# Performance work log

Hardware: AMD Instinct MI355X
Metric: run time of the kernel (lower is better)

Reference implementation:

```python
import jax, jax.numpy as jnp
import numpy as np

EDGE_TYPES = 7
TIME_STEP = 5
STATE_DIM = 1024


def setup_inputs() -> dict:
    key = jax.random.key(0)
    ks = jax.random.split(key, 8)
    B, T, N, DF = 4, 15, 15, 25600
    S, E = STATE_DIM, EDGE_TYPES
    # weights ~ N(0, 0.01), biases zero, matching _initialization()
    return {
        "pose_features": jax.random.normal(ks[0], (B, T, N, DF), jnp.float32),
        "W_compress": jax.random.normal(ks[1], (DF, S), jnp.float32) * 0.01,
        "b_compress": jnp.zeros((S,), jnp.float32),
        "W_edge": jax.random.normal(ks[2], (E, S, S), jnp.float32) * 0.01,
        "b_edge": jnp.zeros((E, S), jnp.float32),
        "W_att": jax.random.normal(ks[3], (E, 2 * S), jnp.float32) * 0.01,
        "b_att": jnp.zeros((E,), jnp.float32),
        "W_r": jax.random.normal(ks[4], (2 * S, S), jnp.float32) * 0.01,
        "b_r": jnp.zeros((S,), jnp.float32),
        "W_z": jax.random.normal(ks[5], (2 * S, S), jnp.float32) * 0.01,
        "b_z": jnp.zeros((S,), jnp.float32),
        "W_h": jax.random.normal(ks[6], (2 * S, S), jnp.float32) * 0.01,
        "b_h": jnp.zeros((S,), jnp.float32),
    }


def reference(pose_features, W_compress, b_compress, W_edge, b_edge,
              W_att, b_att, W_r, b_r, W_z, b_z, W_h, b_h):
    B, T, N, DF = pose_features.shape
    S = W_compress.shape[1]
    E = W_edge.shape[0]
    x = pose_features.reshape(B * T, N, DF)
    prop = x @ W_compress + b_compress                      # [M, N, S]
    # attention Linear over concat(row, col) == row-part + col-part (rank-1 broadcast,
    # avoids materializing the [M, N, N, 2S] repeat/cat tensor; identical math)
    Wa_row, Wa_col = W_att[:, :S], W_att[:, S:]
    scores = None
    for _ in range(1 + TIME_STEP):
        msg = jnp.einsum('bnd,edh->benh', prop, W_edge) + b_edge[None, :, None, :]  # [M,E,N,S]
        row = jnp.einsum('bend,ed->ben', msg, Wa_row)       # [M, E, N]
        col = jnp.einsum('bend,ed->ben', msg, Wa_col)
        scores = jax.nn.sigmoid(row[..., :, None] + col[..., None, :]
                                + b_att[None, :, None, None])   # [M, E, N, N]
        merged = jnp.einsum('beij,bejd->bid', scores, msg)  # [M, N, S]
        a = jnp.concatenate([merged, prop], axis=-1)        # [M, N, 2S]
        r = jax.nn.sigmoid(a @ W_r + b_r)
        z = jax.nn.sigmoid(a @ W_z + b_z)
        h_hat = jnp.tanh(jnp.concatenate([merged, r * prop], axis=-1) @ W_h + b_h)
        prop = (1 - z) * prop + z * h_hat
    box_states = scores.transpose(0, 2, 3, 1)               # [M, N, N, E]
    action_score = ((1 - box_states[..., 0:1]) * box_states).sum(axis=2)
    action_score = action_score.reshape(B, T, N, E)
    actor_score = (1 - box_states[..., 0]).reshape(B, T, N, N)
    acty_score = jax.nn.softmax(
        (action_score * actor_score.sum(axis=-1)[..., None]).sum(axis=2)[:, :, 1:],
        axis=-1)
    return action_score, acty_score, actor_score
```

## Files before the change

kernel.cpp:

```cpp
#include <hip/hip_runtime.h>
#include <hip/hip_bf16.h>

typedef unsigned short bf16_t;
typedef __bf16 bf16x8 __attribute__((ext_vector_type(8)));
typedef float f32x4 __attribute__((ext_vector_type(4)));

__device__ __forceinline__ unsigned short f2bf(float x){
  union { __hip_bfloat16 h; unsigned short u; } c;
  c.h = __float2bfloat16(x);
  return c.u;
}
__device__ __forceinline__ float bf2f(bf16_t u){
  union { unsigned short u; __hip_bfloat16 h; } c;
  c.u = u;
  return __bfloat162float(c.h);
}

#define GL2L(g, l) __builtin_amdgcn_global_load_lds( \
    (const __attribute__((address_space(1))) unsigned int*)(g), \
    (__attribute__((address_space(3))) unsigned int*)(l), 16, 0, 0)

template<int ACT, int MAP>
__global__ __launch_bounds__(256)
void gemm_bf16(const bf16_t* __restrict__ A, int lda,
               const bf16_t* __restrict__ Bt, int ldb,
               float* __restrict__ C, int ldc, size_t csplit,
               const float* __restrict__ bias,
               int M, int N, int K, int Kchunk)
{
  __shared__ __align__(16) bf16_t As[3][128*32];
  __shared__ __align__(16) bf16_t Bs[3][128*32];
  const int tid = threadIdx.x;
  const int w = tid >> 6, lane = tid & 63;
  const int wm = w >> 1, wn = w & 1;
  const int lr = lane & 15, kq = lane >> 4;
  int bcol, brow, bks;
  if (MAP == 0) { bcol = blockIdx.x; brow = blockIdx.y; bks = blockIdx.z; }
  else          { bks = blockIdx.x;  bcol = blockIdx.y; brow = blockIdx.z; }
  const int gm0 = brow * 128, gn0 = bcol * 128;
  const int k0 = bks * Kchunk;
  const int nt = (min(k0 + Kchunk, K) - k0) >> 5;

  const int srow = lane >> 2;
  const int scol = ((lane & 3) ^ ((srow >> 1) & 3)) << 3;
  const int am0 = min(gm0 + w*32 + srow,      M-1);
  const int am1 = min(gm0 + w*32 + 16 + srow, M-1);
  const int bn0 = min(gn0 + w*32 + srow,      N-1);
  const int bn1 = min(gn0 + w*32 + 16 + srow, N-1);
  const bf16_t* Ag0 = A  + (size_t)am0*lda + scol;
  const bf16_t* Ag1 = A  + (size_t)am1*lda + scol;
  const bf16_t* Bg0 = Bt + (size_t)bn0*ldb + scol;
  const bf16_t* Bg1 = Bt + (size_t)bn1*ldb + scol;

  auto STAGEF = [&](int t, int slot) {
    const int kk = k0 + (t << 5);
    char* al = (char*)(&As[slot][0]) + w*2048;
    char* bl = (char*)(&Bs[slot][0]) + w*2048;
    GL2L(Ag0 + kk, al);
    GL2L(Ag1 + kk, al + 1024);
    GL2L(Bg0 + kk, bl);
    GL2L(Bg1 + kk, bl + 1024);
  };

  STAGEF(0, 0);
  if (nt > 1) STAGEF(1, 1);

  const int kqs = kq ^ ((lr >> 1) & 3);
  f32x4 acc[4][4] = {};

  int cs = 0;
  for (int t = 0; t < nt; ++t) {
    if (nt - t >= 2) { asm volatile("s_waitcnt vmcnt(4)" ::: "memory"); }
    else             { asm volatile("s_waitcnt vmcnt(0)" ::: "memory"); }
    __builtin_amdgcn_s_barrier();
    __builtin_amdgcn_sched_barrier(0);
    if (t + 2 < nt) {
      const int s2 = (cs >= 1) ? cs - 1 : cs + 2;
      STAGEF(t + 2, s2);
    }
    const char* Ab = (const char*)(&As[cs][0]);
    const char* Bb = (const char*)(&Bs[cs][0]);
    bf16x8 af[4], bfr[4];
#pragma unroll
    for (int mi = 0; mi < 4; mi++)
      af[mi] = *(const bf16x8*)(Ab + ((wm*64 + mi*16 + lr) << 6) + (kqs << 4));
#pragma unroll
    for (int ni = 0; ni < 4; ni++)
      bfr[ni] = *(const bf16x8*)(Bb + ((wn*64 + ni*16 + lr) << 6) + (kqs << 4));
    __builtin_amdgcn_s_setprio(1);
#pragma unroll
    for (int mi = 0; mi < 4; mi++)
#pragma unroll
      for (int ni = 0; ni < 4; ni++)
        acc[mi][ni] = __builtin_amdgcn_mfma_f32_16x16x32_bf16(af[mi], bfr[ni], acc[mi][ni], 0, 0, 0);
    __builtin_amdgcn_s_setprio(0);
    __builtin_amdgcn_sched_barrier(0);
    cs = (cs == 2) ? 0 : cs + 1;
  }

#pragma unroll
  for (int mi = 0; mi < 4; mi++) {
#pragma unroll
    for (int ni = 0; ni < 4; ni++) {
      const int col = gn0 + wn*64 + ni*16 + lr;
      const float bv = (ACT == 4) ? bias[col] : 0.f;
#pragma unroll
      for (int i = 0; i < 4; i++) {
        const int row = gm0 + wm*64 + mi*16 + kq*4 + i;
        if (row < M) {
          const float v = acc[mi][ni][i] + bv;
          if (ACT == 4) ((bf16_t*)C)[(size_t)row*ldc + col] = f2bf(v);
          else C[(size_t)bks*csplit + (size_t)row*ldc + col] = v;
        }
      }
    }
  }
}

__global__ void reduce_compress(const float* __restrict__ part, const float* __restrict__ bias,
                                float* __restrict__ prop, bf16_t* __restrict__ xr)
{
  const int idx = blockIdx.x*256 + threadIdx.x;
  const int m = idx >> 10, d = idx & 1023;
  float v = bias[d];
#pragma unroll
  for (int z = 0; z < 8; z++) v += part[(size_t)z*921600 + idx];
  prop[idx] = v;
  xr[(size_t)m*2048 + 1024 + d] = f2bf(v);
}

__global__ void reduce_rz(const float* __restrict__ part, const float* __restrict__ bias,
                          const float* __restrict__ prop, float* __restrict__ Zbuf,
                          bf16_t* __restrict__ Xh)
{
  const int idx = blockIdx.x*256 + threadIdx.x;
  const int m = idx >> 11, c = idx & 2047;
  float v = part[idx] + part[1843200 + idx] + bias[c];
  v = 1.f / (1.f + __expf(-v));
  if (c < 1024) Xh[(size_t)m*2048 + 1024 + c] = f2bf(v * prop[(size_t)m*1024 + c]);
  else          Zbuf[(size_t)m*1024 + (c - 1024)] = v;
}

__global__ void reduce_h(const float* __restrict__ part, const float* __restrict__ bias,
                         const float* __restrict__ Zbuf, float* __restrict__ prop,
                         bf16_t* __restrict__ X)
{
  const int idx = blockIdx.x*256 + threadIdx.x;
  const int m = idx >> 10, d = idx & 1023;
  float v = bias[d];
#pragma unroll
  for (int z = 0; z < 4; z++) v += part[(size_t)z*921600 + idx];
  v = tanhf(v);
  const float zz = Zbuf[idx];
  const float pn = (1.f - zz)*prop[idx] + zz*v;
  prop[idx] = pn;
  X[(size_t)m*2048 + 1024 + d] = f2bf(pn);
}

__global__ void compute_u(const float* __restrict__ We, const float* __restrict__ Wa,
                          float* __restrict__ u_row, float* __restrict__ u_col)
{
  const int w = threadIdx.x >> 6, lane = threadIdx.x & 63;
  const int idx = blockIdx.x*4 + w;
  const int e = idx >> 10, h = idx & 1023;
  const float* wep = We + ((size_t)e*1024 + h)*1024;
  const float* wr  = Wa + (size_t)e*2048;
  const float* wc  = wr + 1024;
  float ar = 0.f, ac = 0.f;
#pragma unroll
  for (int t = 0; t < 16; t++) {
    const float v = wep[lane + 64*t];
    ar += v*wr[lane + 64*t];
    ac += v*wc[lane + 64*t];
  }
  for (int off = 32; off; off >>= 1) { ar += __shfl_down(ar, off); ac += __shfl_down(ac, off); }
  if (lane == 0) { u_row[idx] = ar; u_col[idx] = ac; }
}

__global__ void crc_kernel(const float* __restrict__ be, const float* __restrict__ Wa,
                           float* __restrict__ crc)
{
  const int w = threadIdx.x >> 6, lane = threadIdx.x & 63;
  for (int idx = w; idx < 14; idx += 4) {
    const int e = idx >> 1, which = idx & 1;
    const float* bp = be + e*1024;
    const float* wp = Wa + (size_t)e*2048 + which*1024;
    float a = 0.f;
#pragma unroll
    for (int t = 0; t < 16; t++) a += bp[lane + 64*t]*wp[lane + 64*t];
    for (int off = 32; off; off >>= 1) a += __shfl_down(a, off);
    if (lane == 0) crc[which*7 + e] = a;
  }
}

__global__ void attn_kernel(const float* __restrict__ prop, const float* __restrict__ u_row,
                            const float* __restrict__ u_col, const float* __restrict__ crc,
                            const float* __restrict__ b_att, float* __restrict__ scores)
{
  const int b = blockIdx.x, e = blockIdx.y;
  __shared__ float rowv[15], colv[15];
  const int w = threadIdx.x >> 6, lane = threadIdx.x & 63;
  const float* ur = u_row + (size_t)e*1024;
  const float* uc = u_col + (size_t)e*1024;
  for (int n = w; n < 15; n += 4) {
    const float* pr = prop + (size_t)(b*15 + n)*1024;
    float ar = 0.f, ac = 0.f;
#pragma unroll
    for (int t = 0; t < 16; t++) {
      const float pv = pr[lane + 64*t];
      ar += pv*ur[lane + 64*t];
      ac += pv*uc[lane + 64*t];
    }
    for (int off = 32; off; off >>= 1) { ar += __shfl_down(ar, off); ac += __shfl_down(ac, off); }
    if (lane == 0) { rowv[n] = ar; colv[n] = ac; }
  }
  __syncthreads();
  const float base = b_att[e] + crc[e] + crc[7 + e];
  for (int idx = threadIdx.x; idx < 225; idx += 256) {
    const int i = idx/15, j = idx - i*15;
    const float s = 1.f / (1.f + __expf(-(rowv[i] + colv[j] + base)));
    scores[((size_t)(b*7 + e)*15 + i)*15 + j] = s;
  }
}

__global__ void merged_kernel(const bf16_t* __restrict__ msg, const float* __restrict__ scores,
                              bf16_t* __restrict__ X, bf16_t* __restrict__ Xh)
{
  const int b = blockIdx.x, c = blockIdx.y;
  __shared__ float ms[15*7*128];
  __shared__ float sc[1575];
  for (int q = threadIdx.x; q < 3360; q += 256) {
    const int idx = q*4;
    const int j = idx / 896;
    const int rem = idx - j*896;
    const int e = rem >> 7, dl = rem & 127;
    const ushort4 v = *(const ushort4*)(msg + (size_t)(b*15 + j)*7168 + e*1024 + c*128 + dl);
    ms[idx]   = bf2f(v.x);
    ms[idx+1] = bf2f(v.y);
    ms[idx+2] = bf2f(v.z);
    ms[idx+3] = bf2f(v.w);
  }
  for (int idx = threadIdx.x; idx < 1575; idx += 256)
    sc[idx] = scores[(size_t)b*1575 + idx];
  __syncthreads();
  for (int oi = threadIdx.x; oi < 1920; oi += 256) {
    const int i = oi >> 7, dl = oi & 127;
    float acc = 0.f;
#pragma unroll
    for (int e = 0; e < 7; e++)
#pragma unroll
      for (int j = 0; j < 15; j++)
        acc += sc[(e*15 + i)*15 + j] * ms[j*896 + e*128 + dl];
    const bf16_t o = f2bf(acc);
    X [(size_t)(b*15 + i)*2048 + c*128 + dl] = o;
    Xh[(size_t)(b*15 + i)*2048 + c*128 + dl] = o;
  }
}

__global__ void transpose_k(const float* __restrict__ in, bf16_t* __restrict__ out,
                            int R, int C, int out_ld, size_t in_batch, size_t out_batch)
{
  __shared__ float t[64][65];
  in  += (size_t)blockIdx.z * in_batch;
  out += (size_t)blockIdx.z * out_batch;
  const int r0 = blockIdx.x*64, c0 = blockIdx.y*64;
  const int tc = threadIdx.x & 63, tr = threadIdx.x >> 6;
#pragma unroll
  for (int i = 0; i < 16; i++) {
    const int r = tr*16 + i;
    t[r][tc] = in[(size_t)(r0 + r)*C + c0 + tc];
  }
  __syncthreads();
#pragma unroll
  for (int i = 0; i < 16; i++) {
    const int rr = tr*16 + i;
    out[(size_t)(c0 + rr)*out_ld + r0 + tc] = f2bf(t[tc][rr]);
  }
}

__global__ void cast_f32_bf16(const float4* __restrict__ in, ushort4* __restrict__ out, int n4)
{
  int i = blockIdx.x*256 + threadIdx.x;
  const int stride = gridDim.x*256;
  for (; i < n4; i += stride) {
    const float4 v = in[i];
    out[i] = make_ushort4(f2bf(v.x), f2bf(v.y), f2bf(v.z), f2bf(v.w));
  }
}

__global__ void cat2_kernel(const float* __restrict__ a, const float* __restrict__ b,
                            float* __restrict__ o)
{
  const int i = blockIdx.x*256 + threadIdx.x;
  if (i < 1024) o[i] = a[i];
  else if (i < 2048) o[i] = b[i - 1024];
}

__global__ void finalize_kernel(const float* __restrict__ scores, float* __restrict__ out)
{
  const int b = blockIdx.x;
  __shared__ float sc[1575];
  __shared__ float act[105];
  __shared__ float asum[15];
  __shared__ float t2[7];
  for (int idx = threadIdx.x; idx < 1575; idx += 256)
    sc[idx] = scores[(size_t)b*1575 + idx];
  __syncthreads();
  for (int idx = threadIdx.x; idx < 105; idx += 256) {
    const int i = idx/7, e = idx - i*7;
    float a = 0.f;
#pragma unroll
    for (int j = 0; j < 15; j++)
      a += (1.f - sc[i*15 + j]) * sc[(e*15 + i)*15 + j];
    act[idx] = a;
    out[(size_t)b*105 + idx] = a;
  }
  for (int idx = threadIdx.x; idx < 225; idx += 256) {
    const int i = idx/15, j = idx - i*15;
    out[6660 + (size_t)b*225 + idx] = 1.f - sc[i*15 + j];
  }
  if (threadIdx.x < 15) {
    const int i = threadIdx.x;
    float s = 0.f;
#pragma unroll
    for (int j = 0; j < 15; j++) s += 1.f - sc[i*15 + j];
    asum[i] = s;
  }
  __syncthreads();
  if (threadIdx.x < 7) {
    const int e = threadIdx.x;
    float t = 0.f;
#pragma unroll
    for (int i = 0; i < 15; i++) t += act[i*7 + e]*asum[i];
    t2[e] = t;
  }
  __syncthreads();
  if (threadIdx.x == 0) {
    float mx = -1e30f;
    for (int e = 1; e < 7; e++) mx = fmaxf(mx, t2[e]);
    float s = 0.f, ex[6];
    for (int e = 1; e < 7; e++) { ex[e-1] = __expf(t2[e] - mx); s += ex[e-1]; }
    for (int e = 1; e < 7; e++) out[6300 + (size_t)b*6 + (e-1)] = ex[e-1]/s;
  }
}

extern "C" void kernel_launch(void* const* d_in, const int* in_sizes, int n_in,
                              void* d_out, int out_size, void* d_ws, size_t ws_size,
                              hipStream_t stream)
{
  const float* pose = (const float*)d_in[0];
  const float* Wc   = (const float*)d_in[1];
  const float* bc   = (const float*)d_in[2];
  const float* We   = (const float*)d_in[3];
  const float* be   = (const float*)d_in[4];
  const float* Wa   = (const float*)d_in[5];
  const float* ba   = (const float*)d_in[6];
  const float* Wr   = (const float*)d_in[7];
  const float* br   = (const float*)d_in[8];
  const float* Wz   = (const float*)d_in[9];
  const float* bz   = (const float*)d_in[10];
  const float* Wh   = (const float*)d_in[11];
  const float* bh   = (const float*)d_in[12];
  float* out = (float*)d_out;

  char* p = (char*)d_ws;
  auto alloc = [&](size_t b) { char* r = p; p += (b + 255) & ~(size_t)255; return r; };
  bf16_t* Wedge_t = (bf16_t*)alloc(7168ull*1024*2);
  bf16_t* Wrz_t   = (bf16_t*)alloc(2048ull*2048*2);
  bf16_t* Wh_t    = (bf16_t*)alloc(1024ull*2048*2);
  bf16_t* X       = (bf16_t*)alloc(900ull*2048*2);
  float*  prop    = (float*) alloc(900ull*1024*4);
  float*  scores  = (float*) alloc(60ull*7*15*15*4);
  float*  u_row   = (float*) alloc(7168*4);
  float*  u_col   = (float*) alloc(7168*4);
  float*  crc     = (float*) alloc(64);
  float*  brzv    = (float*) alloc(2048*4);
  char* r1 = alloc(128000000ull);
  bf16_t* Abf     = (bf16_t*)r1;
  bf16_t* Wct     = (bf16_t*)(r1 + 46080000ull);
  float*  partial = (float*) (r1 + 46080000ull + 52428800ull);
  bf16_t* msgb    = (bf16_t*)r1;
  float*  Zbuf    = (float*) (r1 + 12902400ull);
  bf16_t* Xh      = (bf16_t*)(r1 + 16588800ull);
  float*  partRZ  = (float*) (r1 + 20275200ull);
  float*  partH   = (float*) (r1 + 49766400ull);

  compute_u<<<1792, 256, 0, stream>>>(We, Wa, u_row, u_col);
  crc_kernel<<<1, 256, 0, stream>>>(be, Wa, crc);
  cast_f32_bf16<<<2048, 256, 0, stream>>>((const float4*)pose, (ushort4*)Abf, 23040000/4);
  transpose_k<<<dim3(400,16,1), 256, 0, stream>>>(Wc, Wct, 25600, 1024, 25600, 0, 0);
  transpose_k<<<dim3(16,16,7),  256, 0, stream>>>(We, Wedge_t, 1024, 1024, 1024,
                                                  1024ull*1024, 1024ull*1024);
  transpose_k<<<dim3(32,16,1),  256, 0, stream>>>(Wr, Wrz_t, 2048, 1024, 2048, 0, 0);
  transpose_k<<<dim3(32,16,1),  256, 0, stream>>>(Wz, Wrz_t + 1024ull*2048, 2048, 1024, 2048, 0, 0);
  transpose_k<<<dim3(32,16,1),  256, 0, stream>>>(Wh, Wh_t, 2048, 1024, 2048, 0, 0);
  cat2_kernel<<<8, 256, 0, stream>>>(br, bz, brzv);

  gemm_bf16<0,1><<<dim3(8,8,8), 256, 0, stream>>>(Abf, 25600, Wct, 25600,
      partial, 1024, 921600ull, nullptr, 900, 1024, 25600, 3200);
  reduce_compress<<<3600, 256, 0, stream>>>(partial, bc, prop, X);

  for (int it = 0; it < 6; it++) {
    attn_kernel<<<dim3(60,7), 256, 0, stream>>>(prop, u_row, u_col, crc, ba, scores);
    if (it == 5) break;
    gemm_bf16<4,0><<<dim3(56,8,1), 256, 0, stream>>>(X + 1024, 2048, Wedge_t, 1024,
        (float*)msgb, 7168, 0, be, 900, 7168, 1024, 1024);
    merged_kernel<<<dim3(60,8), 256, 0, stream>>>(msgb, scores, X, Xh);
    gemm_bf16<0,0><<<dim3(16,8,2), 256, 0, stream>>>(X, 2048, Wrz_t, 2048,
        partRZ, 2048, 1843200ull, nullptr, 900, 2048, 2048, 1024);
    reduce_rz<<<7200, 256, 0, stream>>>(partRZ, brzv, prop, Zbuf, Xh);
    gemm_bf16<0,0><<<dim3(8,8,4), 256, 0, stream>>>(Xh, 2048, Wh_t, 2048,
        partH, 1024, 921600ull, nullptr, 900, 1024, 2048, 512);
    reduce_h<<<3600, 256, 0, stream>>>(partH, bh, Zbuf, prop, X);
  }

  finalize_kernel<<<60, 256, 0, stream>>>(scores, out);
}
```

Measured before the change: 765.9 us.

## Shrink GEMM tile to 128x64 with register-staged double-buffered LDS loads

Rewrites the bf16 GEMM to use 128x64 output tiles instead of 128x128. It replaces the direct global-to-LDS async loads and triple buffering with register-staged loads into a double-buffered LDS, and raises the occupancy hint to 4 blocks per CU. Launch grids double along N to cover the same outputs, so more blocks are available to fill the CUs on these small-M (900) problems. The cost is less reuse of each A tile, which means more A traffic, plus extra VGPRs and LDS write instructions for staging.

```diff
diff --git a/kernel.cpp b/kernel.cpp
--- a/kernel.cpp
+++ b/kernel.cpp
@@ -4,6 +4,7 @@
 typedef unsigned short bf16_t;
 typedef __bf16 bf16x8 __attribute__((ext_vector_type(8)));
 typedef float f32x4 __attribute__((ext_vector_type(4)));
+typedef unsigned short ushort8_t __attribute__((ext_vector_type(8)));
 
 __device__ __forceinline__ unsigned short f2bf(float x){
   union { __hip_bfloat16 h; unsigned short u; } c;
@@ -16,20 +17,16 @@
   return __bfloat162float(c.h);
 }
 
-#define GL2L(g, l) __builtin_amdgcn_global_load_lds( \
-    (const __attribute__((address_space(1))) unsigned int*)(g), \
-    (__attribute__((address_space(3))) unsigned int*)(l), 16, 0, 0)
-
 template<int ACT, int MAP>
-__global__ __launch_bounds__(256)
+__global__ __launch_bounds__(256, 4)
 void gemm_bf16(const bf16_t* __restrict__ A, int lda,
                const bf16_t* __restrict__ Bt, int ldb,
                float* __restrict__ C, int ldc, size_t csplit,
                const float* __restrict__ bias,
                int M, int N, int K, int Kchunk)
 {
-  __shared__ __align__(16) bf16_t As[3][128*32];
-  __shared__ __align__(16) bf16_t Bs[3][128*32];
+  __shared__ __align__(16) bf16_t As[2][128*32];
+  __shared__ __align__(16) bf16_t Bs[2][64*32];
   const int tid = threadIdx.x;
   const int w = tid >> 6, lane = tid & 63;
   const int wm = w >> 1, wn = w & 1;
@@ -37,72 +34,73 @@
   int bcol, brow, bks;
   if (MAP == 0) { bcol = blockIdx.x; brow = blockIdx.y; bks = blockIdx.z; }
   else          { bks = blockIdx.x;  bcol = blockIdx.y; brow = blockIdx.z; }
-  const int gm0 = brow * 128, gn0 = bcol * 128;
+  const int gm0 = brow * 128, gn0 = bcol * 64;
   const int k0 = bks * Kchunk;
   const int nt = (min(k0 + Kchunk, K) - k0) >> 5;
 
-  const int srow = lane >> 2;
-  const int scol = ((lane & 3) ^ ((srow >> 1) & 3)) << 3;
-  const int am0 = min(gm0 + w*32 + srow,      M-1);
-  const int am1 = min(gm0 + w*32 + 16 + srow, M-1);
-  const int bn0 = min(gn0 + w*32 + srow,      N-1);
-  const int bn1 = min(gn0 + w*32 + 16 + srow, N-1);
-  const bf16_t* Ag0 = A  + (size_t)am0*lda + scol;
-  const bf16_t* Ag1 = A  + (size_t)am1*lda + scol;
-  const bf16_t* Bg0 = Bt + (size_t)bn0*ldb + scol;
-  const bf16_t* Bg1 = Bt + (size_t)bn1*ldb + scol;
-
-  auto STAGEF = [&](int t, int slot) {
-    const int kk = k0 + (t << 5);
-    char* al = (char*)(&As[slot][0]) + w*2048;
-    char* bl = (char*)(&Bs[slot][0]) + w*2048;
-    GL2L(Ag0 + kk, al);
-    GL2L(Ag1 + kk, al + 1024);
-    GL2L(Bg0 + kk, bl);
-    GL2L(Bg1 + kk, bl + 1024);
-  };
-
-  STAGEF(0, 0);
-  if (nt > 1) STAGEF(1, 1);
+  const int r0 = tid >> 2, s0 = tid & 3;
+  const int kg0 = s0 ^ ((r0 >> 1) & 3);
+  const int ar0 = min(gm0 + r0,      M-1);
+  const int ar1 = min(gm0 + 64 + r0, M-1);
+  const int br0 = min(gn0 + r0,      N-1);
+  const bf16_t* pA0 = A  + (size_t)ar0*lda + k0 + kg0*8;
+  const bf16_t* pA1 = A  + (size_t)ar1*lda + k0 + kg0*8;
+  const bf16_t* pB0 = Bt + (size_t)br0*ldb + k0 + kg0*8;
+  bf16_t* Al = &As[0][0] + tid*8;
+  bf16_t* Bl = &Bs[0][0] + tid*8;
+  ushort8_t va0, va1, vb0;
+
+#define LDT(t) do { \
+    va0 = *(const ushort8_t*)(pA0 + (size_t)(t)*32); \
+    va1 = *(const ushort8_t*)(pA1 + (size_t)(t)*32); \
+    vb0 = *(const ushort8_t*)(pB0 + (size_t)(t)*32); \
+  } while(0)
+#define WRT(b) do { \
+    *(ushort8_t*)(Al + (b)*4096)        = va0; \
+    *(ushort8_t*)(Al + (b)*4096 + 2048) = va1; \
+    *(ushort8_t*)(Bl + (b)*2048)        = vb0; } while(0)
+
+  LDT(0); WRT(0);
+  if (nt > 1) LDT(1);
+  asm volatile("s_waitcnt lgkmcnt(0)" ::: "memory");
+  __builtin_amdgcn_s_barrier();
+  __builtin_amdgcn_sched_barrier(0);
 
   const int kqs = kq ^ ((lr >> 1) & 3);
-  f32x4 acc[4][4] = {};
-
-  int cs = 0;
+  f32x4 acc[4][2] = {};
+
   for (int t = 0; t < nt; ++t) {
-    if (nt - t >= 2) { asm volatile("s_waitcnt vmcnt(4)" ::: "memory"); }
-    else             { asm volatile("s_waitcnt vmcnt(0)" ::: "memory"); }
+    const int cb = t & 1;
+    const bf16_t* Ab = &As[0][0] + cb*4096;
+    const bf16_t* Bb = &Bs[0][0] + cb*2048;
+    bf16x8 af[4], bfr[2];
+#pragma unroll
+    for (int mi = 0; mi < 4; mi++)
+      af[mi] = *(const bf16x8*)((const char*)Ab + ((wm*64 + mi*16 + lr) << 6) + (kqs << 4));
+#pragma unroll
+    for (int ni = 0; ni < 2; ni++)
+      bfr[ni] = *(const bf16x8*)((const char*)Bb + ((wn*32 + ni*16 + lr) << 6) + (kqs << 4));
+    if (t + 1 < nt) WRT(cb ^ 1);
+    if (t + 2 < nt) LDT(t + 2);
+    __builtin_amdgcn_s_setprio(1);
+#pragma unroll
+    for (int mi = 0; mi < 4; mi++)
+#pragma unroll
+      for (int ni = 0; ni < 2; ni++)
+        acc[mi][ni] = __builtin_amdgcn_mfma_f32_16x16x32_bf16(af[mi], bfr[ni], acc[mi][ni], 0, 0, 0);
+    __builtin_amdgcn_s_setprio(0);
+    asm volatile("s_waitcnt lgkmcnt(0)" ::: "memory");
     __builtin_amdgcn_s_barrier();
     __builtin_amdgcn_sched_barrier(0);
-    if (t + 2 < nt) {
-      const int s2 = (cs >= 1) ? cs - 1 : cs + 2;
-      STAGEF(t + 2, s2);
-    }
-    const char* Ab = (const char*)(&As[cs][0]);
-    const char* Bb = (const char*)(&Bs[cs][0]);
-    bf16x8 af[4], bfr[4];
-#pragma unroll
-    for (int mi = 0; mi < 4; mi++)
-      af[mi] = *(const bf16x8*)(Ab + ((wm*64 + mi*16 + lr) << 6) + (kqs << 4));
-#pragma unroll
-    for (int ni = 0; ni < 4; ni++)
-      bfr[ni] = *(const bf16x8*)(Bb + ((wn*64 + ni*16 + lr) << 6) + (kqs << 4));
-    __builtin_amdgcn_s_setprio(1);
-#pragma unroll
-    for (int mi = 0; mi < 4; mi++)
-#pragma unroll
-      for (int ni = 0; ni < 4; ni++)
-        acc[mi][ni] = __builtin_amdgcn_mfma_f32_16x16x32_bf16(af[mi], bfr[ni], acc[mi][ni], 0, 0, 0);
-    __builtin_amdgcn_s_setprio(0);
-    __builtin_amdgcn_sched_barrier(0);
-    cs = (cs == 2) ? 0 : cs + 1;
-  }
+  }
+#undef LDT
+#undef WRT
 
 #pragma unroll
   for (int mi = 0; mi < 4; mi++) {
 #pragma unroll
-    for (int ni = 0; ni < 4; ni++) {
-      const int col = gn0 + wn*64 + ni*16 + lr;
+    for (int ni = 0; ni < 2; ni++) {
+      const int col = gn0 + wn*32 + ni*16 + lr;
       const float bv = (ACT == 4) ? bias[col] : 0.f;
 #pragma unroll
       for (int i = 0; i < 4; i++) {
@@ -396,20 +394,20 @@
   transpose_k<<<dim3(32,16,1),  256, 0, stream>>>(Wh, Wh_t, 2048, 1024, 2048, 0, 0);
   cat2_kernel<<<8, 256, 0, stream>>>(br, bz, brzv);
 
-  gemm_bf16<0,1><<<dim3(8,8,8), 256, 0, stream>>>(Abf, 25600, Wct, 25600,
+  gemm_bf16<0,1><<<dim3(8,16,8), 256, 0, stream>>>(Abf, 25600, Wct, 25600,
       partial, 1024, 921600ull, nullptr, 900, 1024, 25600, 3200);
   reduce_compress<<<3600, 256, 0, stream>>>(partial, bc, prop, X);
 
   for (int it = 0; it < 6; it++) {
     attn_kernel<<<dim3(60,7), 256, 0, stream>>>(prop, u_row, u_col, crc, ba, scores);
     if (it == 5) break;
-    gemm_bf16<4,0><<<dim3(56,8,1), 256, 0, stream>>>(X + 1024, 2048, Wedge_t, 1024,
+    gemm_bf16<4,0><<<dim3(112,8,1), 256, 0, stream>>>(X + 1024, 2048, Wedge_t, 1024,
         (float*)msgb, 7168, 0, be, 900, 7168, 1024, 1024);
     merged_kernel<<<dim3(60,8), 256, 0, stream>>>(msgb, scores, X, Xh);
-    gemm_bf16<0,0><<<dim3(16,8,2), 256, 0, stream>>>(X, 2048, Wrz_t, 2048,
+    gemm_bf16<0,0><<<dim3(32,8,2), 256, 0, stream>>>(X, 2048, Wrz_t, 2048,
         partRZ, 2048, 1843200ull, nullptr, 900, 2048, 2048, 1024);
     reduce_rz<<<7200, 256, 0, stream>>>(partRZ, brzv, prop, Zbuf, Xh);
-    gemm_bf16<0,0><<<dim3(8,8,4), 256, 0, stream>>>(Xh, 2048, Wh_t, 2048,
+    gemm_bf16<0,0><<<dim3(16,8,4), 256, 0, stream>>>(Xh, 2048, Wh_t, 2048,
         partH, 1024, 921600ull, nullptr, 900, 1024, 2048, 512);
     reduce_h<<<3600, 256, 0, stream>>>(partH, bh, Zbuf, prop, X);
   }
```

After: 700.8 us. 1.09x faster.
